# Performance work log

Measured on AMD Instinct MI355X. Metric: run time of the kernel, lower is better.

## Reference

```python
import jax, jax.numpy as jnp
import numpy as np

N_NODES = 100000
N_EDGES = 1600000
D = 32


def setup_inputs() -> dict:
    key = jax.random.key(0)
    k1, k2, k3, k4, k5, k6, k7 = jax.random.split(key, 7)
    x = jax.random.normal(k1, (N_NODES, D), dtype=jnp.float32)
    edge_index = jax.random.randint(k2, (2, N_EDGES), 0, N_NODES, dtype=jnp.int64)
    edge_weight = jax.random.uniform(k3, (N_EDGES,), dtype=jnp.float32)
    s = 1.0 / np.sqrt(D)
    W1 = jax.random.uniform(k4, (D, D), jnp.float32, -s, s)
    b1 = jax.random.uniform(k5, (D,), jnp.float32, -s, s)
    W2 = jax.random.uniform(k6, (D, D), jnp.float32, -s, s)
    b2 = jax.random.uniform(k7, (D,), jnp.float32, -s, s)
    return {"x": x, "edge_index": edge_index, "edge_weight": edge_weight,
            "W1": W1, "b1": b1, "W2": W2, "b2": b2}


def reference(x, edge_index, edge_weight, W1, b1, W2, b2):
    N = x.shape[0]
    src, dst = edge_index[0], edge_index[1]
    # gcn_norm with improved=True: self-loops get fill value 2.0
    loops = jnp.arange(N, dtype=edge_index.dtype)
    src_a = jnp.concatenate([src, loops])
    dst_a = jnp.concatenate([dst, loops])
    w_a = jnp.concatenate([edge_weight, jnp.full((N,), 2.0, x.dtype)])
    deg = jax.ops.segment_sum(w_a, dst_a, num_segments=N)          # [N]
    dinv = jnp.where(deg > 0, jax.lax.rsqrt(deg), 0.0)             # deg^-1/2, inf->0
    norm = dinv[src_a] * w_a * dinv[dst_a]                          # [E+N]

    def gcn_conv(h, W, b):
        h = h @ W                                                   # [N,D] dense transform
        msg = h[src_a] * norm[:, None]                              # gather + normalize [E+N,D]
        return jax.ops.segment_sum(msg, dst_a, num_segments=N) + b  # scatter-add + bias

    h = jax.nn.relu(gcn_conv(x, W1, b1))
    h = jax.nn.relu(gcn_conv(h, W2, b2))
    # F.dropout treated as identity (deterministic inference reference)
    return h
```

## Files before the change

### kernel.cpp

```cpp
#include <hip/hip_runtime.h>

#define D       32
#define BS      256
#define CBLK    500
#define CBLKP   500
#define BSH     7
#define BNODES  128
#define MAXBUCK 1024
#define MAX_EPT 13
#define ECAP    4096
#define POISON_BASE ((int)0xAAAAAAAAu)

__device__ inline unsigned bf16pack2(float a, float b) {
    unsigned ua = __float_as_uint(a);
    unsigned ub = __float_as_uint(b);
    ua = (ua + 0x7FFFu + ((ua >> 16) & 1)) >> 16;
    ub = (ub + 0x7FFFu + ((ub >> 16) & 1)) >> 16;
    return ua | (ub << 16);
}
__device__ inline uint2 bf16pack4(float4 v) {
    return make_uint2(bf16pack2(v.x, v.y), bf16pack2(v.z, v.w));
}
__device__ inline float4 bf16unpack4(uint2 h) {
    return make_float4(__uint_as_float(h.x << 16),
                       __uint_as_float(h.x & 0xFFFF0000u),
                       __uint_as_float(h.y << 16),
                       __uint_as_float(h.y & 0xFFFF0000u));
}

__global__ void k_localsort_gemm(const int* __restrict__ dst, const int* __restrict__ src,
                                 const float* __restrict__ w, int* __restrict__ bc,
                                 int* __restrict__ locoff, int2* __restrict__ staged,
                                 int E, int EPB, int NBUCK, int NBUCKP,
                                 const float* __restrict__ X, const float* __restrict__ Wm,
                                 uint2* __restrict__ H, int n) {
    __shared__ int    bins[MAXBUCK];
    __shared__ int    sscan[BS];
    __shared__ int    carry;
    __shared__ float4 Ws[D * 8];
    int t = threadIdx.x;

    if ((int)blockIdx.x >= CBLK) {
        for (int i = t; i < D * 8; i += BS) Ws[i] = ((const float4*)Wm)[i];
        __syncthreads();
        int gid  = (blockIdx.x - CBLK) * BS + t;
        int node = gid >> 3;
        int q    = gid & 7;
        if (node >= n) return;
        float4 xv  = ((const float4*)X)[node * 8 + q];
        float4 acc = make_float4(0.f, 0.f, 0.f, 0.f);
#pragma unroll
        for (int k = 0; k < D; ++k) {
            float comp = (k & 3) == 0 ? xv.x : (k & 3) == 1 ? xv.y
                       : (k & 3) == 2 ? xv.z : xv.w;
            float  xk = __shfl(comp, k >> 2, 8);
            float4 wr = Ws[k * 8 + q];
            acc.x += xk * wr.x; acc.y += xk * wr.y;
            acc.z += xk * wr.z; acc.w += xk * wr.w;
        }
        H[node * 8 + q] = bf16pack4(acc);
        return;
    }

    int blk = blockIdx.x;
    int beg = blk * EPB;
    int end = min(E, beg + EPB);
    for (int i = t; i < NBUCK; i += BS) bins[i] = 0;
    __syncthreads();

    int   stash[MAX_EPT];
    int   ssrc[MAX_EPT];
    float swv[MAX_EPT];
#pragma unroll
    for (int i = 0; i < MAX_EPT; ++i) {
        int e = beg + i * BS + t;
        stash[i] = -1;
        if (e < end) {
            int dv = dst[e];
            int b  = dv >> BSH;
            int r  = atomicAdd(&bins[b], 1);
            stash[i] = (b << 12) | r;
            ssrc[i]  = src[e] | ((dv & (BNODES - 1)) << 17);
            swv[i]   = w[e];
        }
    }
    __syncthreads();
    for (int i = t; i < NBUCK; i += BS) bc[blk * NBUCKP + i] = bins[i];
    __syncthreads();
    if (t == 0) carry = 0;
    __syncthreads();
    for (int base = 0; base < NBUCK; base += BS) {
        int idx = base + t;
        int v = (idx < NBUCK) ? bins[idx] : 0;
        sscan[t] = v;
        __syncthreads();
        for (int off = 1; off < BS; off <<= 1) {
            int u = (t >= off) ? sscan[t - off] : 0;
            __syncthreads();
            sscan[t] += u;
            __syncthreads();
        }
        if (idx < NBUCK) bins[idx] = carry + sscan[t] - v;
        __syncthreads();
        if (t == 0) carry += sscan[BS - 1];
        __syncthreads();
    }
    for (int i = t; i < NBUCK; i += BS) locoff[blk * NBUCKP + i] = bins[i];
    __syncthreads();

    int2* myslice = staged + (size_t)blk * EPB;
#pragma unroll
    for (int i = 0; i < MAX_EPT; ++i) {
        if (stash[i] >= 0) {
            int b   = stash[i] >> 12;
            int r   = stash[i] & 0xFFF;
            int pos = bins[b] + r;
            myslice[pos] = make_int2(ssrc[i], __float_as_int(swv[i]));
        }
    }
}

__global__ void k_trans(const int* __restrict__ bc, const int* __restrict__ locoff,
                        int* __restrict__ bcT, int* __restrict__ locoffT,
                        int* __restrict__ btot, int NBUCK, int NBUCKP) {
    __shared__ int tile[32][33];
    const int* in  = (blockIdx.z == 0) ? bc  : locoff;
    int*       out = (blockIdx.z == 0) ? bcT : locoffT;
    int c0 = blockIdx.x * 32;
    int r0 = blockIdx.y * 32;
    int tx = threadIdx.x & 31, ty = threadIdx.x >> 5;
    for (int dy = ty; dy < 32; dy += 8) {
        int r = r0 + dy, c = c0 + tx;
        tile[dy][tx] = (r < CBLK && c < NBUCK) ? in[r * NBUCKP + c] : 0;
    }
    __syncthreads();
    for (int dy = ty; dy < 32; dy += 8) {
        int c = c0 + dy, r = r0 + tx;
        if (c < NBUCK && r < CBLK) out[c * CBLKP + r] = tile[tx][dy];
    }
    if (blockIdx.z == 0 && ty == 0 && c0 + tx < NBUCK) {
        int s = 0;
#pragma unroll
        for (int dy = 0; dy < 32; ++dy) s += tile[dy][tx];
        if (s) atomicAdd(&btot[c0 + tx], s);
    }
}

__global__ void k_merge(const int* __restrict__ bcT, const int* __restrict__ locoffT,
                        const int* __restrict__ btot, const int2* __restrict__ staged,
                        int2* __restrict__ emeta, int* __restrict__ rowptr,
                        float* __restrict__ dinv, uint2* __restrict__ H,
                        int N, int E, int NBUCK, int EPB) {
    __shared__ int2  ebuf[ECAP];
    __shared__ int   runoff[CBLK];
    __shared__ int   lrun[CBLK];
    __shared__ int   sscan[BS];
    __shared__ int   carry;
    __shared__ int   ihist[BNODES];
    __shared__ float fdeg[BNODES];
    __shared__ int   cursor[BNODES];
    __shared__ float sdinv[BNODES];
    __shared__ int   wsum;
    __shared__ int   bstart_s;
    int b = blockIdx.x, t = threadIdx.x;

    {
        int pacc = 0;
        for (int k = t; k < b; k += BS) pacc += btot[k];
        sscan[t] = pacc;
        __syncthreads();
        for (int off = BS / 2; off > 0; off >>= 1) {
            if (t < off) sscan[t] += sscan[t + off];
            __syncthreads();
        }
        if (t == 0) bstart_s = sscan[0];
        __syncthreads();
    }
    int bstart = bstart_s;

    for (int k = t; k < CBLK; k += BS) {
        runoff[k] = bcT[b * CBLKP + k];
        lrun[k]   = locoffT[b * CBLKP + k];
    }
    if (t < BNODES) { ihist[t] = 0; fdeg[t] = 0.0f; }
    if (t == 0) carry = 0;
    __syncthreads();
    for (int base = 0; base < CBLK; base += BS) {
        int idx = base + t;
        int v = (idx < CBLK) ? runoff[idx] : 0;
        sscan[t] = v;
        __syncthreads();
        for (int off = 1; off < BS; off <<= 1) {
            int u = (t >= off) ? sscan[t - off] : 0;
            __syncthreads();
            sscan[t] += u;
            __syncthreads();
        }
        if (idx < CBLK) runoff[idx] = carry + sscan[t] - v;
        __syncthreads();
        if (t == 0) carry += sscan[BS - 1];
        __syncthreads();
    }
    int total = carry;
    bool fits = total <= ECAP;

    for (int k = t; k < CBLK; k += BS) {
        int gs = runoff[k];
        int ge = (k + 1 < CBLK) ? runoff[k + 1] : total;
        const int2* run = staged + (size_t)k * EPB + lrun[k];
        for (int j = 0; j < ge - gs; ++j) {
            int2 v = run[j];
            int local = (v.x >> 17) & (BNODES - 1);
            atomicAdd(&ihist[local], 1);
            atomicAdd(&fdeg[local], __int_as_float(v.y));
            if (fits) ebuf[gs + j] = v;
        }
    }
    __syncthreads();
    int v128 = 0, incl = 0;
    if (t < BNODES) {
        v128 = ihist[t];
        incl = v128;
#pragma unroll
        for (int off = 1; off < 64; off <<= 1) {
            int u = __shfl_up(incl, off, 64);
            if ((t & 63) >= off) incl += u;
        }
    }
    if (t == 63) wsum = incl;
    __syncthreads();
    if (t < BNODES) {
        if (t >= 64) incl += wsum;
        int excl = incl - v128;
        int node = b * BNODES + t;
        float di = rsqrtf(2.0f + fdeg[t]);
        if (node < N) {
            rowptr[node] = bstart + excl;
            dinv[node]   = di;
        }
        sdinv[t]  = di;
        cursor[t] = excl;
    }
    if (b == NBUCK - 1 && t == 0) rowptr[N] = E;
    __syncthreads();
    {
        int base_node = b * BNODES;
        for (int i = t; i < BNODES * 8; i += BS) {
            int row  = i >> 3;
            int node = base_node + row;
            if (node < N) {
                float di = sdinv[row];
                size_t off = (size_t)node * 8 + (i & 7);
                float4 f = bf16unpack4(H[off]);
                f.x *= di; f.y *= di; f.z *= di; f.w *= di;
                H[off] = bf16pack4(f);
            }
        }
    }
    __syncthreads();
    for (int k = t; k < CBLK; k += BS) {
        int gs = runoff[k];
        int ge = (k + 1 < CBLK) ? runoff[k + 1] : total;
        const int2* run = staged + (size_t)k * EPB + lrun[k];
        for (int j = 0; j < ge - gs; ++j) {
            int2 v = fits ? ebuf[gs + j] : run[j];
            int local = (v.x >> 17) & (BNODES - 1);
            int r = atomicAdd(&cursor[local], 1);
            emeta[bstart + r] = make_int2(v.x & 0x1FFFF, v.y);
        }
    }
}

template <bool FUSE_GEMM>
__global__ void k_agg(const int* __restrict__ rowptr, const int2* __restrict__ emeta,
                      const uint4* __restrict__ Hs, const float* __restrict__ dinv,
                      const float* __restrict__ b, const float* __restrict__ W2,
                      void* __restrict__ outv, int n) {
    __shared__ float4 Ws[D * 8];
    int tid = threadIdx.x;
    if (FUSE_GEMM) {
        for (int i = tid; i < D * 8; i += BS) Ws[i] = ((const float4*)W2)[i];
        __syncthreads();
    }

    int gid  = blockIdx.x * BS + tid;
    int node = gid >> 2;
    int q    = gid & 3;
    if (node >= n) return;

    float  di  = dinv[node];
    float4 bq0 = ((const float4*)b)[q * 2];
    float4 bq1 = ((const float4*)b)[q * 2 + 1];
    uint4  h0  = Hs[node * 4 + q];
    float4 a0  = bf16unpack4(make_uint2(h0.x, h0.y));
    float4 a1  = bf16unpack4(make_uint2(h0.z, h0.w));
    float4 acc0 = make_float4(2.f * a0.x, 2.f * a0.y, 2.f * a0.z, 2.f * a0.w);
    float4 acc1 = make_float4(2.f * a1.x, 2.f * a1.y, 2.f * a1.z, 2.f * a1.w);

    int beg  = rowptr[node];
    int end  = rowptr[node + 1];
    int full = beg + ((end - beg) & ~7);

    for (int i0 = beg; i0 < full; i0 += 8) {
        int2 em0 = emeta[i0 + q];
        int2 em1 = emeta[i0 + 4 + q];
        float nm0 = __int_as_float(em0.y);
        float nm1 = __int_as_float(em1.y);
#pragma unroll
        for (int j = 0; j < 4; ++j) {
            int   s  = __shfl(em0.x, j, 4);
            float nm = __shfl(nm0, j, 4);
            uint4 hv = Hs[s * 4 + q];
            float4 f0 = bf16unpack4(make_uint2(hv.x, hv.y));
            float4 f1 = bf16unpack4(make_uint2(hv.z, hv.w));
            acc0.x += nm * f0.x; acc0.y += nm * f0.y; acc0.z += nm * f0.z; acc0.w += nm * f0.w;
            acc1.x += nm * f1.x; acc1.y += nm * f1.y; acc1.z += nm * f1.z; acc1.w += nm * f1.w;
        }
#pragma unroll
        for (int j = 0; j < 4; ++j) {
            int   s  = __shfl(em1.x, j, 4);
            float nm = __shfl(nm1, j, 4);
            uint4 hv = Hs[s * 4 + q];
            float4 f0 = bf16unpack4(make_uint2(hv.x, hv.y));
            float4 f1 = bf16unpack4(make_uint2(hv.z, hv.w));
            acc0.x += nm * f0.x; acc0.y += nm * f0.y; acc0.z += nm * f0.z; acc0.w += nm * f0.w;
            acc1.x += nm * f1.x; acc1.y += nm * f1.y; acc1.z += nm * f1.z; acc1.w += nm * f1.w;
        }
    }
    if (full < end) {
        int idx0 = full + q;
        int idx1 = full + 4 + q;
        int2 em0 = (idx0 < end) ? emeta[idx0] : make_int2(0, 0);
        int2 em1 = (idx1 < end) ? emeta[idx1] : make_int2(0, 0);
        float nm0 = (idx0 < end) ? __int_as_float(em0.y) : 0.0f;
        float nm1 = (idx1 < end) ? __int_as_float(em1.y) : 0.0f;
        int rem = end - full;
        int r0 = rem < 4 ? rem : 4;
        for (int j = 0; j < r0; ++j) {
            int   s  = __shfl(em0.x, j, 4);
            float nm = __shfl(nm0, j, 4);
            uint4 hv = Hs[s * 4 + q];
            float4 f0 = bf16unpack4(make_uint2(hv.x, hv.y));
            float4 f1 = bf16unpack4(make_uint2(hv.z, hv.w));
            acc0.x += nm * f0.x; acc0.y += nm * f0.y; acc0.z += nm * f0.z; acc0.w += nm * f0.w;
            acc1.x += nm * f1.x; acc1.y += nm * f1.y; acc1.z += nm * f1.z; acc1.w += nm * f1.w;
        }
        for (int j = 0; j < rem - 4; ++j) {
            int   s  = __shfl(em1.x, j, 4);
            float nm = __shfl(nm1, j, 4);
            uint4 hv = Hs[s * 4 + q];
            float4 f0 = bf16unpack4(make_uint2(hv.x, hv.y));
            float4 f1 = bf16unpack4(make_uint2(hv.z, hv.w));
            acc0.x += nm * f0.x; acc0.y += nm * f0.y; acc0.z += nm * f0.z; acc0.w += nm * f0.w;
            acc1.x += nm * f1.x; acc1.y += nm * f1.y; acc1.z += nm * f1.z; acc1.w += nm * f1.w;
        }
    }
    acc0.x = fmaxf(di * acc0.x + bq0.x, 0.f);
    acc0.y = fmaxf(di * acc0.y + bq0.y, 0.f);
    acc0.z = fmaxf(di * acc0.z + bq0.z, 0.f);
    acc0.w = fmaxf(di * acc0.w + bq0.w, 0.f);
    acc1.x = fmaxf(di * acc1.x + bq1.x, 0.f);
    acc1.y = fmaxf(di * acc1.y + bq1.y, 0.f);
    acc1.z = fmaxf(di * acc1.z + bq1.z, 0.f);
    acc1.w = fmaxf(di * acc1.w + bq1.w, 0.f);

    if (FUSE_GEMM) {
        float4 o0 = make_float4(0.f, 0.f, 0.f, 0.f);
        float4 o1 = make_float4(0.f, 0.f, 0.f, 0.f);
#pragma unroll
        for (int k = 0; k < D; ++k) {
            int sel = k & 7;
            float comp = sel == 0 ? acc0.x : sel == 1 ? acc0.y : sel == 2 ? acc0.z
                       : sel == 3 ? acc0.w : sel == 4 ? acc1.x : sel == 5 ? acc1.y
                       : sel == 6 ? acc1.z : acc1.w;
            float  hk = __shfl(comp, k >> 3, 4);
            float4 w0 = Ws[k * 8 + q * 2];
            float4 w1 = Ws[k * 8 + q * 2 + 1];
            o0.x += hk * w0.x; o0.y += hk * w0.y; o0.z += hk * w0.z; o0.w += hk * w0.w;
            o1.x += hk * w1.x; o1.y += hk * w1.y; o1.z += hk * w1.z; o1.w += hk * w1.w;
        }
        o0.x *= di; o0.y *= di; o0.z *= di; o0.w *= di;
        o1.x *= di; o1.y *= di; o1.z *= di; o1.w *= di;
        ((uint4*)outv)[node * 4 + q] =
            make_uint4(bf16pack2(o0.x, o0.y), bf16pack2(o0.z, o0.w),
                       bf16pack2(o1.x, o1.y), bf16pack2(o1.z, o1.w));
    } else {
        ((float4*)outv)[node * 8 + q * 2]     = acc0;
        ((float4*)outv)[node * 8 + q * 2 + 1] = acc1;
    }
}

__global__ void k_hist_gemm(const int4* __restrict__ dst4, int* __restrict__ cnt,
                            int4* __restrict__ rank4, int E4,
                            const float* __restrict__ X, const float* __restrict__ W,
                            uint2* __restrict__ H, int n, int gE4) {
    __shared__ float4 Ws[D * 8];
    int tid = threadIdx.x;
    if ((int)blockIdx.x < gE4) {
        int i = blockIdx.x * BS + tid;
        if (i >= E4) return;
        int4 d = dst4[i];
        int4 r;
        r.x = atomicAdd(&cnt[d.x], 1) - POISON_BASE;
        r.y = atomicAdd(&cnt[d.y], 1) - POISON_BASE;
        r.z = atomicAdd(&cnt[d.z], 1) - POISON_BASE;
        r.w = atomicAdd(&cnt[d.w], 1) - POISON_BASE;
        rank4[i] = r;
        return;
    }
    for (int i = tid; i < D * 8; i += BS) Ws[i] = ((const float4*)W)[i];
    __syncthreads();
    int gid  = (blockIdx.x - gE4) * BS + tid;
    int node = gid >> 3;
    int q    = gid & 7;
    if (node >= n) return;
    float4 xv  = ((const float4*)X)[node * 8 + q];
    float4 acc = make_float4(0.f, 0.f, 0.f, 0.f);
#pragma unroll
    for (int k = 0; k < D; ++k) {
        float comp = (k & 3) == 0 ? xv.x : (k & 3) == 1 ? xv.y
                   : (k & 3) == 2 ? xv.z : xv.w;
        float  xk = __shfl(comp, k >> 2, 8);
        float4 wr = Ws[k * 8 + q];
        acc.x += xk * wr.x; acc.y += xk * wr.y;
        acc.z += xk * wr.z; acc.w += xk * wr.w;
    }
    H[node * 8 + q] = bf16pack4(acc);
}

__global__ void k_scan1(const int* __restrict__ cnt, int* __restrict__ bsum, int n) {
    __shared__ int s[BS];
    int t = threadIdx.x, i = blockIdx.x * BS + t;
    s[t] = (i < n) ? (cnt[i] - POISON_BASE) : 0;
    __syncthreads();
    for (int off = BS / 2; off > 0; off >>= 1) {
        if (t < off) s[t] += s[t + off];
        __syncthreads();
    }
    if (t == 0) bsum[blockIdx.x] = s[0];
}

__global__ void k_scan23(const int* __restrict__ cnt, const int* __restrict__ bsum,
                         int* __restrict__ rowptr, int n) {
    __shared__ int red[BS];
    __shared__ int s[BS];
    int t = threadIdx.x, i = blockIdx.x * BS + t;
    int pacc = 0;
    for (int k = t; k < (int)blockIdx.x; k += BS) pacc += bsum[k];
    red[t] = pacc;
    __syncthreads();
    for (int off = BS / 2; off > 0; off >>= 1) {
        if (t < off) red[t] += red[t + off];
        __syncthreads();
    }
    int bpre = red[0];
    int v = (i < n) ? (cnt[i] - POISON_BASE) : 0;
    s[t] = v;
    __syncthreads();
    for (int off = 1; off < BS; off <<= 1) {
        int u = (t >= off) ? s[t - off] : 0;
        __syncthreads();
        s[t] += u;
        __syncthreads();
    }
    if (i < n) {
        int excl = bpre + s[t] - v;
        rowptr[i] = excl;
        if (i == n - 1) rowptr[n] = excl + v;
    }
}

__global__ void k_reorder(const int4* __restrict__ src4, const int4* __restrict__ dst4,
                          const float4* __restrict__ w4, const int4* __restrict__ rank4,
                          const int* __restrict__ rowptr, int2* __restrict__ emeta, int E4) {
    int i = blockIdx.x * blockDim.x + threadIdx.x;
    if (i >= E4) return;
    int4   s = src4[i];
    int4   d = dst4[i];
    float4 w = w4[i];
    int4   r = rank4[i];
    emeta[rowptr[d.x] + r.x] = make_int2(s.x, __float_as_int(w.x));
    emeta[rowptr[d.y] + r.y] = make_int2(s.y, __float_as_int(w.y));
    emeta[rowptr[d.z] + r.z] = make_int2(s.z, __float_as_int(w.z));
    emeta[rowptr[d.w] + r.w] = make_int2(s.w, __float_as_int(w.w));
}

__global__ void k_degscaleF(const int* __restrict__ rowptr, const int2* __restrict__ emeta,
                            float* __restrict__ dinv, uint2* __restrict__ H, int n) {
    int gid  = blockIdx.x * blockDim.x + threadIdx.x;
    int node = gid >> 3;
    int c    = gid & 7;
    if (node >= n) return;
    int beg = rowptr[node], end = rowptr[node + 1];
    float sum = 0.0f;
    for (int idx = beg + c; idx < end; idx += 8)
        sum += __int_as_float(emeta[idx].y);
    sum += __shfl_xor(sum, 4, 8);
    sum += __shfl_xor(sum, 2, 8);
    sum += __shfl_xor(sum, 1, 8);
    float di = rsqrtf(2.0f + sum);
    if (c == 0) dinv[node] = di;
    di = __shfl(di, 0, 8);
    size_t off = (size_t)node * 8 + c;
    float4 f = bf16unpack4(H[off]);
    f.x *= di; f.y *= di; f.z *= di; f.w *= di;
    H[off] = bf16pack4(f);
}

extern "C" void kernel_launch(void* const* d_in, const int* in_sizes, int n_in,
                              void* d_out, int out_size, void* d_ws, size_t ws_size,
                              hipStream_t stream) {
    const float* x   = (const float*)d_in[0];
    const int*   ei  = (const int*)d_in[1];
    const float* w   = (const float*)d_in[2];
    const float* W1  = (const float*)d_in[3];
    const float* b1  = (const float*)d_in[4];
    const float* W2  = (const float*)d_in[5];
    const float* b2  = (const float*)d_in[6];
    float*       out = (float*)d_out;

    const int N = in_sizes[0] / D;
    const int E = in_sizes[2];
    const int* src = ei;
    const int* dst = ei + E;

    const int NBUCK  = (N + BNODES - 1) / BNODES;
    const int NBUCKP = (NBUCK + 3) & ~3;
    const int EPB    = (E + CBLK - 1) / CBLK;
    const int NB     = (N + BS - 1) / BS;
    const int E4     = E / 4;
    const int gE4    = (E4 + BS - 1) / BS;
    const int gN8    = (N * 8 + BS - 1) / BS;
    const int gN4    = (N * 4 + BS - 1) / BS;

    char*  base    = (char*)d_ws;
    int2*  emeta   = (int2*)base;
    uint2* ht      = (uint2*)(base + (size_t)E * 8);
    uint2* ht2     = ht + (size_t)N * 8;
    float* dinv    = (float*)(ht2 + (size_t)N * 8);
    int*   rowptr  = (int*)(dinv + N);
    int2*  staged  = (int2*)(rowptr + ((N + 4) & ~3));
    int*   bc      = (int*)(staged + E);
    int*   locoff  = bc + (size_t)CBLK * NBUCKP;
    int*   bcT     = locoff + (size_t)CBLK * NBUCKP;
    int*   locoffT = bcT + (size_t)NBUCK * CBLKP;
    int*   btot    = locoffT + (size_t)NBUCK * CBLKP;
    size_t need    = (size_t)((char*)(btot + NBUCKP) - base);

    bool main_ok = (ws_size >= need) && (NBUCK <= MAXBUCK) && (N < (1 << 17)) &&
                   ((EPB + BS - 1) / BS <= MAX_EPT) && (EPB <= 4096) && (N % 4 == 0);

    if (main_ok) {
        hipMemsetAsync(btot, 0, (size_t)NBUCKP * 4, stream);
        k_localsort_gemm<<<CBLK + gN8, BS, 0, stream>>>(dst, src, w, bc, locoff, staged,
                                                        E, EPB, NBUCK, NBUCKP, x, W1, ht, N);
        dim3 tg((NBUCK + 31) / 32, (CBLK + 31) / 32, 2);
        k_trans<<<tg, BS, 0, stream>>>(bc, locoff, bcT, locoffT, btot, NBUCK, NBUCKP);
        k_merge<<<NBUCK, BS, 0, stream>>>(bcT, locoffT, btot, staged, emeta, rowptr, dinv,
                                          ht, N, E, NBUCK, EPB);
        k_agg<true ><<<gN4, BS, 0, stream>>>(rowptr, emeta, (const uint4*)ht,  dinv, b1, W2, ht2, N);
        k_agg<false><<<gN4, BS, 0, stream>>>(rowptr, emeta, (const uint4*)ht2, dinv, b2, nullptr, out, N);
    } else {
        int* cnt  = (int*)staged;
        int* rank = cnt + N;
        int* bsum = rank + E;
        k_hist_gemm<<<gE4 + gN8, BS, 0, stream>>>((const int4*)dst, cnt, (int4*)rank, E4,
                                                  x, W1, ht, N, gE4);
        k_scan1 <<<NB, BS, 0, stream>>>(cnt, bsum, N);
        k_scan23<<<NB, BS, 0, stream>>>(cnt, bsum, rowptr, N);
        k_reorder<<<(E4 + BS - 1) / BS, BS, 0, stream>>>((const int4*)src, (const int4*)dst,
                                                         (const float4*)w, (const int4*)rank,
                                                         rowptr, emeta, E4);
        k_degscaleF<<<gN8, BS, 0, stream>>>(rowptr, emeta, dinv, ht, N);
        k_agg<true ><<<gN4, BS, 0, stream>>>(rowptr, emeta, (const uint4*)ht,  dinv, b1, W2, ht2, N);
        k_agg<false><<<gN4, BS, 0, stream>>>(rowptr, emeta, (const uint4*)ht2, dinv, b2, nullptr, out, N);
    }
}
```

Baseline: 197.3 us.

## Stage local sort in LDS, use wave-shuffle scans, flatten merge loops

The local-sort kernel now counts buckets in one pass, then re-reads edges and scatters them into a shared-memory buffer, so the global write of the staged slice becomes a coalesced linear copy instead of per-thread register stashes with scattered stores. The barrier-heavy Hillis-Steele LDS scans are replaced by a wave-shuffle scan helper, and the prefix over bucket totals uses a shuffle reduction. In the merge kernel, the per-run serial loops are replaced by a flat per-edge loop that finds each edge's source run by binary search, which balances work across threads. The cost is reading dst twice plus extra shared memory and binary-search work per edge.

```diff
diff --git a/kernel.cpp b/kernel.cpp
--- a/kernel.cpp
+++ b/kernel.cpp
@@ -7,7 +7,7 @@
 #define BSH     7
 #define BNODES  128
 #define MAXBUCK 1024
-#define MAX_EPT 13
+#define SBUF_CAP 3584
 #define ECAP    4096
 #define POISON_BASE ((int)0xAAAAAAAAu)
 
@@ -26,6 +26,32 @@
                        __uint_as_float(h.x & 0xFFFF0000u),
                        __uint_as_float(h.y << 16),
                        __uint_as_float(h.y & 0xFFFF0000u));
+}
+
+__device__ inline int lds_excl_scan(int* arr, int L, int* wsum, int t) {
+    int carryv = 0;
+    for (int base = 0; base < L; base += BS) {
+        int idx = base + t;
+        int v = (idx < L) ? arr[idx] : 0;
+        int incl = v;
+#pragma unroll
+        for (int off = 1; off < 64; off <<= 1) {
+            int u = __shfl_up(incl, off, 64);
+            if ((t & 63) >= off) incl += u;
+        }
+        if ((t & 63) == 63) wsum[t >> 6] = incl;
+        __syncthreads();
+        int myw = t >> 6;
+        int wpre = 0;
+        if (myw > 0) wpre += wsum[0];
+        if (myw > 1) wpre += wsum[1];
+        if (myw > 2) wpre += wsum[2];
+        int tot = wsum[0] + wsum[1] + wsum[2] + wsum[3];
+        if (idx < L) arr[idx] = carryv + wpre + incl - v;
+        __syncthreads();
+        carryv += tot;
+    }
+    return carryv;
 }
 
 __global__ void k_localsort_gemm(const int* __restrict__ dst, const int* __restrict__ src,
@@ -35,8 +61,8 @@
                                  const float* __restrict__ X, const float* __restrict__ Wm,
                                  uint2* __restrict__ H, int n) {
     __shared__ int    bins[MAXBUCK];
-    __shared__ int    sscan[BS];
-    __shared__ int    carry;
+    __shared__ int    wsum[4];
+    __shared__ int2   sbuf[SBUF_CAP];
     __shared__ float4 Ws[D * 8];
     int t = threadIdx.x;
 
@@ -65,59 +91,28 @@
     int blk = blockIdx.x;
     int beg = blk * EPB;
     int end = min(E, beg + EPB);
+    int cnt = end - beg;
     for (int i = t; i < NBUCK; i += BS) bins[i] = 0;
     __syncthreads();
 
-    int   stash[MAX_EPT];
-    int   ssrc[MAX_EPT];
-    float swv[MAX_EPT];
-#pragma unroll
-    for (int i = 0; i < MAX_EPT; ++i) {
-        int e = beg + i * BS + t;
-        stash[i] = -1;
-        if (e < end) {
-            int dv = dst[e];
-            int b  = dv >> BSH;
-            int r  = atomicAdd(&bins[b], 1);
-            stash[i] = (b << 12) | r;
-            ssrc[i]  = src[e] | ((dv & (BNODES - 1)) << 17);
-            swv[i]   = w[e];
-        }
-    }
+    for (int e = beg + t; e < end; e += BS)
+        atomicAdd(&bins[dst[e] >> BSH], 1);
     __syncthreads();
     for (int i = t; i < NBUCK; i += BS) bc[blk * NBUCKP + i] = bins[i];
     __syncthreads();
-    if (t == 0) carry = 0;
-    __syncthreads();
-    for (int base = 0; base < NBUCK; base += BS) {
-        int idx = base + t;
-        int v = (idx < NBUCK) ? bins[idx] : 0;
-        sscan[t] = v;
-        __syncthreads();
-        for (int off = 1; off < BS; off <<= 1) {
-            int u = (t >= off) ? sscan[t - off] : 0;
-            __syncthreads();
-            sscan[t] += u;
-            __syncthreads();
-        }
-        if (idx < NBUCK) bins[idx] = carry + sscan[t] - v;
-        __syncthreads();
-        if (t == 0) carry += sscan[BS - 1];
-        __syncthreads();
-    }
+    lds_excl_scan(bins, NBUCK, wsum, t);
     for (int i = t; i < NBUCK; i += BS) locoff[blk * NBUCKP + i] = bins[i];
     __syncthreads();
 
+    for (int e = beg + t; e < end; e += BS) {
+        int dv  = dst[e];
+        int b   = dv >> BSH;
+        int pos = atomicAdd(&bins[b], 1);
+        sbuf[pos] = make_int2(src[e] | ((dv & (BNODES - 1)) << 17), __float_as_int(w[e]));
+    }
+    __syncthreads();
     int2* myslice = staged + (size_t)blk * EPB;
-#pragma unroll
-    for (int i = 0; i < MAX_EPT; ++i) {
-        if (stash[i] >= 0) {
-            int b   = stash[i] >> 12;
-            int r   = stash[i] & 0xFFF;
-            int pos = bins[b] + r;
-            myslice[pos] = make_int2(ssrc[i], __float_as_int(swv[i]));
-        }
-    }
+    for (int i = t; i < cnt; i += BS) myslice[i] = sbuf[i];
 }
 
 __global__ void k_trans(const int* __restrict__ bc, const int* __restrict__ locoff,
@@ -154,66 +149,56 @@
     __shared__ int2  ebuf[ECAP];
     __shared__ int   runoff[CBLK];
     __shared__ int   lrun[CBLK];
-    __shared__ int   sscan[BS];
-    __shared__ int   carry;
+    __shared__ int   wsum[4];
     __shared__ int   ihist[BNODES];
     __shared__ float fdeg[BNODES];
     __shared__ int   cursor[BNODES];
     __shared__ float sdinv[BNODES];
-    __shared__ int   wsum;
-    __shared__ int   bstart_s;
+    __shared__ int   hsum;
     int b = blockIdx.x, t = threadIdx.x;
-
-    {
-        int pacc = 0;
-        for (int k = t; k < b; k += BS) pacc += btot[k];
-        sscan[t] = pacc;
-        __syncthreads();
-        for (int off = BS / 2; off > 0; off >>= 1) {
-            if (t < off) sscan[t] += sscan[t + off];
-            __syncthreads();
-        }
-        if (t == 0) bstart_s = sscan[0];
-        __syncthreads();
-    }
-    int bstart = bstart_s;
 
     for (int k = t; k < CBLK; k += BS) {
         runoff[k] = bcT[b * CBLKP + k];
         lrun[k]   = locoffT[b * CBLKP + k];
     }
     if (t < BNODES) { ihist[t] = 0; fdeg[t] = 0.0f; }
-    if (t == 0) carry = 0;
-    __syncthreads();
-    for (int base = 0; base < CBLK; base += BS) {
-        int idx = base + t;
-        int v = (idx < CBLK) ? runoff[idx] : 0;
-        sscan[t] = v;
-        __syncthreads();
-        for (int off = 1; off < BS; off <<= 1) {
-            int u = (t >= off) ? sscan[t - off] : 0;
-            __syncthreads();
-            sscan[t] += u;
-            __syncthreads();
-        }
-        if (idx < CBLK) runoff[idx] = carry + sscan[t] - v;
-        __syncthreads();
-        if (t == 0) carry += sscan[BS - 1];
-        __syncthreads();
-    }
-    int total = carry;
+
+    int pacc = 0;
+    for (int k = t; k < b; k += BS) pacc += btot[k];
+#pragma unroll
+    for (int off = 32; off; off >>= 1) pacc += __shfl_down(pacc, off, 64);
+    if ((t & 63) == 0) wsum[t >> 6] = pacc;
+    __syncthreads();
+    int bstart = wsum[0] + wsum[1] + wsum[2] + wsum[3];
+    __syncthreads();
+
+    int total = lds_excl_scan(runoff, CBLK, wsum, t);
     bool fits = total <= ECAP;
 
-    for (int k = t; k < CBLK; k += BS) {
-        int gs = runoff[k];
-        int ge = (k + 1 < CBLK) ? runoff[k + 1] : total;
-        const int2* run = staged + (size_t)k * EPB + lrun[k];
-        for (int j = 0; j < ge - gs; ++j) {
-            int2 v = run[j];
+    if (fits) {
+        for (int p = t; p < total; p += BS) {
+            int lo = 0, hi = CBLK - 1;
+            while (lo < hi) {
+                int mid = (lo + hi + 1) >> 1;
+                if (runoff[mid] <= p) lo = mid; else hi = mid - 1;
+            }
+            int2 v = staged[(size_t)lo * EPB + lrun[lo] + (p - runoff[lo])];
             int local = (v.x >> 17) & (BNODES - 1);
             atomicAdd(&ihist[local], 1);
             atomicAdd(&fdeg[local], __int_as_float(v.y));
-            if (fits) ebuf[gs + j] = v;
+            ebuf[p] = v;
+        }
+    } else {
+        for (int k = t; k < CBLK; k += BS) {
+            int gs = runoff[k];
+            int ge = (k + 1 < CBLK) ? runoff[k + 1] : total;
+            const int2* run = staged + (size_t)k * EPB + lrun[k];
+            for (int j = 0; j < ge - gs; ++j) {
+                int2 v = run[j];
+                int local = (v.x >> 17) & (BNODES - 1);
+                atomicAdd(&ihist[local], 1);
+                atomicAdd(&fdeg[local], __int_as_float(v.y));
+            }
         }
     }
     __syncthreads();
@@ -227,10 +212,10 @@
             if ((t & 63) >= off) incl += u;
         }
     }
-    if (t == 63) wsum = incl;
+    if (t == 63) hsum = incl;
     __syncthreads();
     if (t < BNODES) {
-        if (t >= 64) incl += wsum;
+        if (t >= 64) incl += hsum;
         int excl = incl - v128;
         int node = b * BNODES + t;
         float di = rsqrtf(2.0f + fdeg[t]);
@@ -258,15 +243,24 @@
         }
     }
     __syncthreads();
-    for (int k = t; k < CBLK; k += BS) {
-        int gs = runoff[k];
-        int ge = (k + 1 < CBLK) ? runoff[k + 1] : total;
-        const int2* run = staged + (size_t)k * EPB + lrun[k];
-        for (int j = 0; j < ge - gs; ++j) {
-            int2 v = fits ? ebuf[gs + j] : run[j];
+    if (fits) {
+        for (int p = t; p < total; p += BS) {
+            int2 v = ebuf[p];
             int local = (v.x >> 17) & (BNODES - 1);
             int r = atomicAdd(&cursor[local], 1);
             emeta[bstart + r] = make_int2(v.x & 0x1FFFF, v.y);
+        }
+    } else {
+        for (int k = t; k < CBLK; k += BS) {
+            int gs = runoff[k];
+            int ge = (k + 1 < CBLK) ? runoff[k + 1] : total;
+            const int2* run = staged + (size_t)k * EPB + lrun[k];
+            for (int j = 0; j < ge - gs; ++j) {
+                int2 v = run[j];
+                int local = (v.x >> 17) & (BNODES - 1);
+                int r = atomicAdd(&cursor[local], 1);
+                emeta[bstart + r] = make_int2(v.x & 0x1FFFF, v.y);
+            }
         }
     }
 }
@@ -548,7 +542,7 @@
     size_t need    = (size_t)((char*)(btot + NBUCKP) - base);
 
     bool main_ok = (ws_size >= need) && (NBUCK <= MAXBUCK) && (N < (1 << 17)) &&
-                   ((EPB + BS - 1) / BS <= MAX_EPT) && (EPB <= 4096) && (N % 4 == 0);
+                   (EPB <= SBUF_CAP) && (N % 4 == 0);
 
     if (main_ok) {
         hipMemsetAsync(btot, 0, (size_t)NBUCKP * 4, stream);
```

Result: faster. 191.4 us (-2.9%).
